# Kernel optimization log

Measured on AMD Instinct MI355X. Metric: run time of the kernel, lower is better.

## Reference

```python
import jax, jax.numpy as jnp
import numpy as np

NUM_HEAD = 16
DIM_MODEL = 1024
DIM_HEAD = DIM_MODEL // NUM_HEAD


def setup_inputs() -> dict:
    key = jax.random.key(0)
    ks = jax.random.split(key, 11)
    B, S, D = 2, 2048, DIM_MODEL
    w = lambda k: jax.random.normal(k, (D, D), dtype=jnp.float32) * 0.02
    b = lambda k: jax.random.normal(k, (D,), dtype=jnp.float32) * 0.02
    return {
        "Q": jax.random.normal(ks[0], (B, S, D), dtype=jnp.float32),
        "K": jax.random.normal(ks[1], (B, S, D), dtype=jnp.float32),
        "V": jax.random.normal(ks[2], (B, S, D), dtype=jnp.float32),
        "WQ": w(ks[3]), "bQ": b(ks[4]),
        "WK": w(ks[5]), "bK": b(ks[6]),
        "WV": w(ks[7]), "bV": b(ks[8]),
        "WO": w(ks[9]), "bO": b(ks[10]),
    }


def reference(Q, K, V, WQ, bQ, WK, bK, WV, bV, WO, bO):
    B, LQ, D = Q.shape
    LK, LV = K.shape[1], V.shape[1]
    H, dh = NUM_HEAD, DIM_HEAD
    # linear projections (torch Linear: x @ W.T + b)
    q = (Q @ WQ.T + bQ).reshape(B, H, LQ, dh)  # NOTE: raw reshape, no transpose (faithful to source)
    k = (K @ WK.T + bK).reshape(B, H, LK, dh)
    v = (V @ WV.T + bV).reshape(B, H, LV, dh)
    # scores: Q @ K^T, scaled by (dim_head ** 1) / 2 == dh/2 (faithful to source precedence)
    scores = jnp.einsum('bhqd,bhkd->bhqk', q, k) / (dh / 2)
    dist = jax.nn.softmax(scores, axis=-1)          # [B,H,LQ,LK]
    attn = jnp.einsum('bhqk,bhkd->bhqd', dist, v)   # [B,H,LQ,dh]
    attn = attn.reshape(B, LQ, H * dh)
    out = attn @ WO.T + bO
    return out, dist
```

## Files before the change

### kernel.cpp

```cpp
#include <hip/hip_runtime.h>
#include <stdint.h>

#define B_ 2
#define S_ 2048
#define D_ 1024
#define H_ 16
#define DH 64
#define BS_ (B_*S_)
#define QBLK 128
#define KBLK 128

typedef unsigned short u16;
typedef __attribute__((ext_vector_type(8))) __bf16 bf16x8;
typedef __attribute__((ext_vector_type(4))) float f32x4;

__device__ __forceinline__ u16 f2bf(float f){
  unsigned u = __float_as_uint(f);
  u += 0x7fffu + ((u >> 16) & 1u);
  return (u16)(u >> 16);
}
__device__ __forceinline__ float bf2f(u16 v){
  return __uint_as_float(((unsigned)v) << 16);
}

union pk8 { u16 a[8]; uint4 v; };

typedef __attribute__((address_space(1))) const unsigned gas_u32;
typedef __attribute__((address_space(3))) unsigned las_u32;
__device__ __forceinline__ void gload16(const void* g, void* l){
  __builtin_amdgcn_global_load_lds((gas_u32*)g, (las_u32*)l, 16, 0, 0);
}

__global__ __launch_bounds__(256) void cvt_kernel(
    const float* __restrict__ Q, const float* __restrict__ K, const float* __restrict__ V,
    const float* __restrict__ WQ, const float* __restrict__ WK,
    const float* __restrict__ WV, const float* __restrict__ WO,
    u16* Qc, u16* Kc, u16* Vc, u16* wq, u16* wk, u16* wv, u16* wo)
{
  const int b = blockIdx.x;
  const float* s; u16* d; size_t off;
  if (b < 6144){
    int t = b >> 11;
    s = t==0?Q:(t==1?K:V); d = t==0?Qc:(t==1?Kc:Vc);
    off = (size_t)(b & 2047)*2048;
  } else {
    int t = (b - 6144) >> 9;
    s = t==0?WQ:(t==1?WK:(t==2?WV:WO)); d = t==0?wq:(t==1?wk:(t==2?wv:wo));
    off = (size_t)((b - 6144) & 511)*2048;
  }
  const float* sp = s + off + (size_t)threadIdx.x*8;
  f32x4 v0 = __builtin_nontemporal_load((const f32x4*)sp);
  f32x4 v1 = __builtin_nontemporal_load((const f32x4*)(sp + 4));
  pk8 p;
  p.a[0]=f2bf(v0[0]); p.a[1]=f2bf(v0[1]); p.a[2]=f2bf(v0[2]); p.a[3]=f2bf(v0[3]);
  p.a[4]=f2bf(v1[0]); p.a[5]=f2bf(v1[1]); p.a[6]=f2bf(v1[2]); p.a[7]=f2bf(v1[3]);
  *(uint4*)(d + off + (size_t)threadIdx.x*8) = p.v;
}

template<int F32OUT>
__device__ __forceinline__ void gemm_body(
    const u16* __restrict__ A, const u16* __restrict__ Wt,
    const float* __restrict__ bias, void* __restrict__ Cout,
    int bm, int bn, int N, int K)
{
  const int tid = threadIdx.x, w = tid >> 6, lane = tid & 63;
  const int g = lane >> 4, c16 = lane & 15;
  const int wr = w >> 1, wc = w & 1;
  const int lr = lane >> 3, lg = lane & 7;
  const int gsrc = lg ^ (lr & 7);

  __shared__ alignas(16) u16 at[2][128*64];
  __shared__ alignas(16) u16 bt[2][128*64];

  f32x4 acc[4][4];
  #pragma unroll
  for (int mi = 0; mi < 4; ++mi)
    #pragma unroll
    for (int ni = 0; ni < 4; ++ni) acc[mi][ni] = (f32x4){0.f,0.f,0.f,0.f};

  auto stage = [&](int buf, int kt){
    #pragma unroll
    for (int i = 0; i < 4; ++i){
      const int r = w*32 + i*8 + lr;
      gload16(A + (size_t)(bm*128 + r)*K + kt + gsrc*8, at[buf] + (w*32 + i*8)*64);
    }
    #pragma unroll
    for (int i = 0; i < 4; ++i){
      const int r = w*32 + i*8 + lr;
      gload16(Wt + (size_t)(bn*128 + r)*K + kt + gsrc*8, bt[buf] + (w*32 + i*8)*64);
    }
  };

  stage(0, 0);
  __syncthreads();
  int cur = 0;
  for (int kt = 0; kt < K; kt += 64){
    if (kt + 64 < K) stage(cur ^ 1, kt + 64);
    #pragma unroll
    for (int ks = 0; ks < 2; ++ks){
      bf16x8 af[4], bfr[4];
      #pragma unroll
      for (int mi = 0; mi < 4; ++mi){
        const int row = wr*64 + mi*16 + c16;
        af[mi] = *(const bf16x8*)(at[cur] + row*64 + ((ks*4 + g) ^ (row & 7))*8);
      }
      #pragma unroll
      for (int ni = 0; ni < 4; ++ni){
        const int row = wc*64 + ni*16 + c16;
        bfr[ni] = *(const bf16x8*)(bt[cur] + row*64 + ((ks*4 + g) ^ (row & 7))*8);
      }
      #pragma unroll
      for (int mi = 0; mi < 4; ++mi)
        #pragma unroll
        for (int ni = 0; ni < 4; ++ni)
          acc[mi][ni] = __builtin_amdgcn_mfma_f32_16x16x32_bf16(
              af[mi], bfr[ni], acc[mi][ni], 0, 0, 0);
    }
    __syncthreads();
    cur ^= 1;
  }

  #pragma unroll
  for (int mi = 0; mi < 4; ++mi){
    const int row0 = bm*128 + wr*64 + mi*16 + g*4;
    #pragma unroll
    for (int ni = 0; ni < 4; ++ni){
      const int col = bn*128 + wc*64 + ni*16 + c16;
      const float bb = bias[col];
      #pragma unroll
      for (int r = 0; r < 4; ++r){
        float v = acc[mi][ni][r] + bb;
        if (F32OUT) __builtin_nontemporal_store(v, (float*)Cout + (size_t)(row0 + r)*N + col);
        else        ((u16*)Cout)[(size_t)(row0 + r)*N + col] = f2bf(v);
      }
    }
  }
}

__global__ __launch_bounds__(256) void qkv_gemm_kernel(
    const u16* __restrict__ A0, const u16* __restrict__ A1, const u16* __restrict__ A2,
    const u16* __restrict__ W0, const u16* __restrict__ W1, const u16* __restrict__ W2,
    const float* __restrict__ b0, const float* __restrict__ b1, const float* __restrict__ b2,
    u16* C0, u16* C1, u16* C2)
{
  const int t = blockIdx.z;
  const u16* A = t==0?A0:(t==1?A1:A2);
  const u16* W = t==0?W0:(t==1?W1:W2);
  const float* bb = t==0?b0:(t==1?b1:b2);
  u16* C = t==0?C0:(t==1?C1:C2);
  gemm_body<0>(A, W, bb, C, blockIdx.x, blockIdx.y, D_, D_);
}

__global__ __launch_bounds__(256) void out_gemm_kernel(
    const u16* __restrict__ A, const u16* __restrict__ W,
    const float* __restrict__ bias, float* __restrict__ C)
{
  gemm_body<1>(A, W, bias, C, blockIdx.x, blockIdx.y, D_, D_);
}

__global__ __launch_bounds__(256) void vtrans_kernel(
    const u16* __restrict__ vb, u16* __restrict__ vtb)
{
  const int kt = blockIdx.x, bh = blockIdx.y;
  __shared__ alignas(16) u16 t[64][80];
  const int tid = threadIdx.x;
  const u16* slab = vb + (size_t)bh*S_*DH + (size_t)kt*64*DH;
  #pragma unroll
  for (int j = 0; j < 2; ++j){
    const int r = j*32 + (tid >> 3), c = (tid & 7)*8;
    *(bf16x8*)(&t[r][c]) = *(const bf16x8*)(slab + (size_t)r*DH + c);
  }
  __syncthreads();
  u16* oslab = vtb + (size_t)bh*DH*S_ + (size_t)kt*64;
  #pragma unroll
  for (int j = 0; j < 2; ++j){
    const int dd = j*32 + (tid >> 3), k8 = (tid & 7)*8;
    pk8 u;
    #pragma unroll
    for (int e = 0; e < 8; ++e) u.a[e] = t[k8 + e][dd];
    *(uint4*)(oslab + (size_t)dd*S_ + k8) = u.v;
  }
}

__global__ __launch_bounds__(512, 4) void attn_kernel(
    const u16* __restrict__ qb, const u16* __restrict__ kb,
    const u16* __restrict__ vtb, float* __restrict__ dist,
    u16* __restrict__ attnb)
{
  const int vb_ = (blockIdx.x & 7)*64 + (blockIdx.x >> 3);
  const int qblk = vb_ & 15, bh = vb_ >> 4;

  const int tid = threadIdx.x, w = tid >> 6, lane = tid & 63;
  const int g = lane >> 4, c16 = lane & 15;
  const int lr = lane >> 3, lg = lane & 7;
  const int gsrc = lg ^ (lr & 7);
  const int lr4 = lane >> 4, lg4 = lane & 15;

  __shared__ alignas(16) u16 klds[128*64];
  __shared__ alignas(16) u16 vtlds[64*128];
  __shared__ alignas(16) u16 plds[8*16*128];

  const u16* qsl = qb  + (size_t)bh*S_*DH;
  const u16* ksl = kb  + (size_t)bh*S_*DH;
  const u16* vsl = vtb + (size_t)bh*DH*S_;

  const int q0 = qblk*QBLK + w*16;
  bf16x8 qf[2];
  #pragma unroll
  for (int ks = 0; ks < 2; ++ks)
    qf[ks] = *(const bf16x8*)(qsl + (size_t)(q0 + c16)*DH + ks*32 + g*8);

  const float cl = (1.0f/32.0f)*1.44269504f;
  float sum = 0.f;

  auto stageK = [&](int kt){
    #pragma unroll
    for (int i = 0; i < 2; ++i){
      const int r = w*16 + i*8 + lr;
      gload16(ksl + (size_t)(kt + r)*DH + gsrc*8, klds + (w*16 + i*8)*64);
    }
  };
  auto stageV = [&](int kt){
    #pragma unroll
    for (int i = 0; i < 2; ++i){
      const int d = w*8 + i*4 + lr4;
      const int gs = lg4 ^ (d & 15);
      gload16(vsl + (size_t)d*S_ + kt + gs*8, vtlds + (w*8 + i*4)*128);
    }
  };

  for (int kt = 0; kt < S_; kt += KBLK){
    stageK(kt);
    __syncthreads();
    #pragma unroll
    for (int ng = 0; ng < 2; ++ng){
      bf16x8 kf[4][2];
      f32x4 s[4];
      #pragma unroll
      for (int j = 0; j < 4; ++j){
        const int krow = (ng*4 + j)*16 + c16;
        kf[j][0] = *(const bf16x8*)(klds + krow*64 + ((0 + g) ^ (krow & 7))*8);
        kf[j][1] = *(const bf16x8*)(klds + krow*64 + ((4 + g) ^ (krow & 7))*8);
      }
      __builtin_amdgcn_s_setprio(1);
      #pragma unroll
      for (int j = 0; j < 4; ++j){
        s[j] = (f32x4){0.f,0.f,0.f,0.f};
        s[j] = __builtin_amdgcn_mfma_f32_16x16x32_bf16(kf[j][0], qf[0], s[j], 0, 0, 0);
      }
      #pragma unroll
      for (int j = 0; j < 4; ++j)
        s[j] = __builtin_amdgcn_mfma_f32_16x16x32_bf16(kf[j][1], qf[1], s[j], 0, 0, 0);
      __builtin_amdgcn_s_setprio(0);
      #pragma unroll
      for (int j = 0; j < 4; ++j)
        #pragma unroll
        for (int r = 0; r < 4; ++r) sum += exp2f(s[j][r]*cl);
    }
    __syncthreads();
  }
  sum += __shfl_xor(sum, 16, 64);
  sum += __shfl_xor(sum, 32, 64);
  const float inv = 1.0f/sum;

  f32x4 oacc[4];
  #pragma unroll
  for (int n2 = 0; n2 < 4; ++n2) oacc[n2] = (f32x4){0.f,0.f,0.f,0.f};

  float* drow0 = dist + ((size_t)bh*S_ + q0)*S_;
  const int rlane = lane >> 5;
  const int chunk = lane & 31;
  const int slotc = chunk >> 1, halfc = (chunk & 1)*4;

  for (int kt = 0; kt < S_; kt += KBLK){
    stageK(kt);
    stageV(kt);
    __syncthreads();
    #pragma unroll
    for (int ng = 0; ng < 2; ++ng){
      bf16x8 kf[4][2];
      f32x4 s[4];
      #pragma unroll
      for (int j = 0; j < 4; ++j){
        const int krow = (ng*4 + j)*16 + c16;
        kf[j][0] = *(const bf16x8*)(klds + krow*64 + ((0 + g) ^ (krow & 7))*8);
        kf[j][1] = *(const bf16x8*)(klds + krow*64 + ((4 + g) ^ (krow & 7))*8);
      }
      __builtin_amdgcn_s_setprio(1);
      #pragma unroll
      for (int j = 0; j < 4; ++j){
        s[j] = (f32x4){0.f,0.f,0.f,0.f};
        s[j] = __builtin_amdgcn_mfma_f32_16x16x32_bf16(kf[j][0], qf[0], s[j], 0, 0, 0);
      }
      #pragma unroll
      for (int j = 0; j < 4; ++j)
        s[j] = __builtin_amdgcn_mfma_f32_16x16x32_bf16(kf[j][1], qf[1], s[j], 0, 0, 0);
      __builtin_amdgcn_s_setprio(0);
      #pragma unroll
      for (int j = 0; j < 4; ++j){
        const int n = ng*4 + j;
        float p0 = exp2f(s[j][0]*cl)*inv, p1 = exp2f(s[j][1]*cl)*inv;
        float p2 = exp2f(s[j][2]*cl)*inv, p3 = exp2f(s[j][3]*cl)*inv;
        const int col = n*16 + g*4;
        const int slot = (col >> 3) ^ c16;
        unsigned lo = (unsigned)f2bf(p0) | ((unsigned)f2bf(p1) << 16);
        unsigned hi = (unsigned)f2bf(p2) | ((unsigned)f2bf(p3) << 16);
        uint2 pk2; pk2.x = lo; pk2.y = hi;
        *(uint2*)(plds + w*2048 + c16*128 + slot*8 + (g & 1)*4) = pk2;
      }
    }
    #pragma unroll
    for (int it = 0; it < 8; ++it){
      const int row = it*2 + rlane;
      const u16* src = plds + w*2048 + row*128 + (slotc ^ row)*8 + halfc;
      uint2 pv = *(const uint2*)src;
      f32x4 o;
      o[0] = bf2f((u16)(pv.x & 0xffffu));
      o[1] = bf2f((u16)(pv.x >> 16));
      o[2] = bf2f((u16)(pv.y & 0xffffu));
      o[3] = bf2f((u16)(pv.y >> 16));
      __builtin_nontemporal_store(o, (f32x4*)(drow0 + (size_t)row*S_ + kt + chunk*4));
    }
    #pragma unroll
    for (int kc = 0; kc < 4; ++kc){
      bf16x8 pf = *(const bf16x8*)(plds + w*2048 + c16*128 + ((kc*4 + g) ^ c16)*8);
      __builtin_amdgcn_s_setprio(1);
      #pragma unroll
      for (int n2 = 0; n2 < 4; ++n2){
        const int d = n2*16 + c16;
        bf16x8 vf = *(const bf16x8*)(vtlds + d*128 + ((kc*4 + g) ^ (d & 15))*8);
        oacc[n2] = __builtin_amdgcn_mfma_f32_16x16x32_bf16(pf, vf, oacc[n2], 0, 0, 0);
      }
      __builtin_amdgcn_s_setprio(0);
    }
    __syncthreads();
  }

  u16* asl = attnb + (size_t)bh*S_*DH;
  #pragma unroll
  for (int n2 = 0; n2 < 4; ++n2)
    #pragma unroll
    for (int r = 0; r < 4; ++r)
      __builtin_nontemporal_store(f2bf(oacc[n2][r]),
          asl + (size_t)(q0 + g*4 + r)*DH + n2*16 + c16);
}

extern "C" void kernel_launch(void* const* d_in, const int* in_sizes, int n_in,
                              void* d_out, int out_size, void* d_ws, size_t ws_size,
                              hipStream_t stream)
{
  const float* Q  = (const float*)d_in[0];
  const float* K  = (const float*)d_in[1];
  const float* V  = (const float*)d_in[2];
  const float* WQ = (const float*)d_in[3]; const float* bQ = (const float*)d_in[4];
  const float* WK = (const float*)d_in[5]; const float* bK = (const float*)d_in[6];
  const float* WV = (const float*)d_in[7]; const float* bV = (const float*)d_in[8];
  const float* WO = (const float*)d_in[9]; const float* bO = (const float*)d_in[10];

  float* out  = (float*)d_out;
  float* dist = out + (size_t)BS_*D_;

  char* ws = (char*)d_ws;
  u16* qb    = (u16*)(ws);
  u16* kb    = (u16*)(ws + (8u<<20));
  u16* vb    = (u16*)(ws + (16u<<20));
  u16* vtb   = (u16*)(ws + (24u<<20));
  u16* attnb = (u16*)(ws + (32u<<20));
  u16* Qc    = (u16*)(ws + (40u<<20));
  u16* Kc    = (u16*)(ws + (48u<<20));
  u16* Vc    = (u16*)(ws + (56u<<20));
  u16* wqb   = (u16*)(ws + (64u<<20));
  u16* wkb   = (u16*)(ws + (66u<<20));
  u16* wvb   = (u16*)(ws + (68u<<20));
  u16* wob   = (u16*)(ws + (70u<<20));

  cvt_kernel<<<8192, 256, 0, stream>>>(Q, K, V, WQ, WK, WV, WO,
                                       Qc, Kc, Vc, wqb, wkb, wvb, wob);

  qkv_gemm_kernel<<<dim3(BS_/128, D_/128, 3), 256, 0, stream>>>(
      Qc, Kc, Vc, wqb, wkb, wvb, bQ, bK, bV, qb, kb, vb);

  vtrans_kernel<<<dim3(S_/64, B_*H_), 256, 0, stream>>>(vb, vtb);

  attn_kernel<<<dim3((S_/QBLK)*(B_*H_)), 512, 0, stream>>>(qb, kb, vtb, dist, attnb);

  out_gemm_kernel<<<dim3(BS_/128, D_/128), 256, 0, stream>>>(attnb, wob, bO, out);
}
```

Before: 230.8 us.

## Fuse fp32-to-bf16 activation conversion into QKV GEMM A-tile loading

The separate conversion pass over Q, K and V is removed. The QKV GEMM now loads fp32 activation tiles into registers, converts them to bf16, and writes them swizzled into LDS, with the next tile's loads overlapping the current MFMA loop. This drops a full fp32 read and bf16 write/read round trip of the activations, at the cost of more registers and re-reading fp32 A once per N-block (8 times) instead of bf16.

```diff
diff --git a/kernel.cpp b/kernel.cpp
--- a/kernel.cpp
+++ b/kernel.cpp
@@ -32,22 +32,15 @@
 }
 
 __global__ __launch_bounds__(256) void cvt_kernel(
-    const float* __restrict__ Q, const float* __restrict__ K, const float* __restrict__ V,
     const float* __restrict__ WQ, const float* __restrict__ WK,
     const float* __restrict__ WV, const float* __restrict__ WO,
-    u16* Qc, u16* Kc, u16* Vc, u16* wq, u16* wk, u16* wv, u16* wo)
+    u16* wq, u16* wk, u16* wv, u16* wo)
 {
   const int b = blockIdx.x;
-  const float* s; u16* d; size_t off;
-  if (b < 6144){
-    int t = b >> 11;
-    s = t==0?Q:(t==1?K:V); d = t==0?Qc:(t==1?Kc:Vc);
-    off = (size_t)(b & 2047)*2048;
-  } else {
-    int t = (b - 6144) >> 9;
-    s = t==0?WQ:(t==1?WK:(t==2?WV:WO)); d = t==0?wq:(t==1?wk:(t==2?wv:wo));
-    off = (size_t)((b - 6144) & 511)*2048;
-  }
+  const int t = b >> 9;
+  const float* s = t==0?WQ:(t==1?WK:(t==2?WV:WO));
+  u16* d = t==0?wq:(t==1?wk:(t==2?wv:wo));
+  const size_t off = (size_t)(b & 511)*2048;
   const float* sp = s + off + (size_t)threadIdx.x*8;
   f32x4 v0 = __builtin_nontemporal_load((const f32x4*)sp);
   f32x4 v1 = __builtin_nontemporal_load((const f32x4*)(sp + 4));
@@ -57,9 +50,9 @@
   *(uint4*)(d + off + (size_t)threadIdx.x*8) = p.v;
 }
 
-template<int F32OUT>
+template<int F32OUT, int AF32>
 __device__ __forceinline__ void gemm_body(
-    const u16* __restrict__ A, const u16* __restrict__ Wt,
+    const void* __restrict__ Ap, const u16* __restrict__ Wt,
     const float* __restrict__ bias, void* __restrict__ Cout,
     int bm, int bn, int N, int K)
 {
@@ -78,12 +71,35 @@
     #pragma unroll
     for (int ni = 0; ni < 4; ++ni) acc[mi][ni] = (f32x4){0.f,0.f,0.f,0.f};
 
-  auto stage = [&](int buf, int kt){
+  f32x4 a0[4], a1[4];
+  auto loadA = [&](int kt){
+    #pragma unroll
+    for (int i = 0; i < 4; ++i){
+      const int id = tid + i*256, row = id >> 3, gi = id & 7;
+      const float* src = (const float*)Ap + (size_t)(bm*128 + row)*K + kt + gi*8;
+      a0[i] = __builtin_nontemporal_load((const f32x4*)src);
+      a1[i] = __builtin_nontemporal_load((const f32x4*)(src + 4));
+    }
+  };
+  auto writeA = [&](int buf){
+    #pragma unroll
+    for (int i = 0; i < 4; ++i){
+      const int id = tid + i*256, row = id >> 3, gi = id & 7;
+      pk8 p;
+      p.a[0]=f2bf(a0[i][0]); p.a[1]=f2bf(a0[i][1]); p.a[2]=f2bf(a0[i][2]); p.a[3]=f2bf(a0[i][3]);
+      p.a[4]=f2bf(a1[i][0]); p.a[5]=f2bf(a1[i][1]); p.a[6]=f2bf(a1[i][2]); p.a[7]=f2bf(a1[i][3]);
+      *(uint4*)(at[buf] + row*64 + ((gi ^ (row & 7)))*8) = p.v;
+    }
+  };
+  auto stageA = [&](int buf, int kt){
     #pragma unroll
     for (int i = 0; i < 4; ++i){
       const int r = w*32 + i*8 + lr;
-      gload16(A + (size_t)(bm*128 + r)*K + kt + gsrc*8, at[buf] + (w*32 + i*8)*64);
-    }
+      gload16((const u16*)Ap + (size_t)(bm*128 + r)*K + kt + gsrc*8,
+              at[buf] + (w*32 + i*8)*64);
+    }
+  };
+  auto stageB = [&](int buf, int kt){
     #pragma unroll
     for (int i = 0; i < 4; ++i){
       const int r = w*32 + i*8 + lr;
@@ -91,11 +107,16 @@
     }
   };
 
-  stage(0, 0);
+  if (AF32){ loadA(0); stageB(0, 0); writeA(0); }
+  else     { stageA(0, 0); stageB(0, 0); }
   __syncthreads();
   int cur = 0;
   for (int kt = 0; kt < K; kt += 64){
-    if (kt + 64 < K) stage(cur ^ 1, kt + 64);
+    const bool more = kt + 64 < K;
+    if (more){
+      if (AF32) loadA(kt + 64); else stageA(cur ^ 1, kt + 64);
+      stageB(cur ^ 1, kt + 64);
+    }
     #pragma unroll
     for (int ks = 0; ks < 2; ++ks){
       bf16x8 af[4], bfr[4];
@@ -116,6 +137,7 @@
           acc[mi][ni] = __builtin_amdgcn_mfma_f32_16x16x32_bf16(
               af[mi], bfr[ni], acc[mi][ni], 0, 0, 0);
     }
+    if (AF32 && more) writeA(cur ^ 1);
     __syncthreads();
     cur ^= 1;
   }
@@ -138,24 +160,24 @@
 }
 
 __global__ __launch_bounds__(256) void qkv_gemm_kernel(
-    const u16* __restrict__ A0, const u16* __restrict__ A1, const u16* __restrict__ A2,
+    const float* __restrict__ Q, const float* __restrict__ K, const float* __restrict__ V,
     const u16* __restrict__ W0, const u16* __restrict__ W1, const u16* __restrict__ W2,
     const float* __restrict__ b0, const float* __restrict__ b1, const float* __restrict__ b2,
     u16* C0, u16* C1, u16* C2)
 {
   const int t = blockIdx.z;
-  const u16* A = t==0?A0:(t==1?A1:A2);
+  const float* A = t==0?Q:(t==1?K:V);
   const u16* W = t==0?W0:(t==1?W1:W2);
   const float* bb = t==0?b0:(t==1?b1:b2);
   u16* C = t==0?C0:(t==1?C1:C2);
-  gemm_body<0>(A, W, bb, C, blockIdx.x, blockIdx.y, D_, D_);
+  gemm_body<0,1>(A, W, bb, C, blockIdx.x, blockIdx.y, D_, D_);
 }
 
 __global__ __launch_bounds__(256) void out_gemm_kernel(
     const u16* __restrict__ A, const u16* __restrict__ W,
     const float* __restrict__ bias, float* __restrict__ C)
 {
-  gemm_body<1>(A, W, bias, C, blockIdx.x, blockIdx.y, D_, D_);
+  gemm_body<1,0>(A, W, bias, C, blockIdx.x, blockIdx.y, D_, D_);
 }
 
 __global__ __launch_bounds__(256) void vtrans_kernel(
@@ -366,19 +388,15 @@
   u16* vb    = (u16*)(ws + (16u<<20));
   u16* vtb   = (u16*)(ws + (24u<<20));
   u16* attnb = (u16*)(ws + (32u<<20));
-  u16* Qc    = (u16*)(ws + (40u<<20));
-  u16* Kc    = (u16*)(ws + (48u<<20));
-  u16* Vc    = (u16*)(ws + (56u<<20));
-  u16* wqb   = (u16*)(ws + (64u<<20));
-  u16* wkb   = (u16*)(ws + (66u<<20));
-  u16* wvb   = (u16*)(ws + (68u<<20));
-  u16* wob   = (u16*)(ws + (70u<<20));
-
-  cvt_kernel<<<8192, 256, 0, stream>>>(Q, K, V, WQ, WK, WV, WO,
-                                       Qc, Kc, Vc, wqb, wkb, wvb, wob);
+  u16* wqb   = (u16*)(ws + (40u<<20));
+  u16* wkb   = (u16*)(ws + (42u<<20));
+  u16* wvb   = (u16*)(ws + (44u<<20));
+  u16* wob   = (u16*)(ws + (46u<<20));
+
+  cvt_kernel<<<2048, 256, 0, stream>>>(WQ, WK, WV, WO, wqb, wkb, wvb, wob);
 
   qkv_gemm_kernel<<<dim3(BS_/128, D_/128, 3), 256, 0, stream>>>(
-      Qc, Kc, Vc, wqb, wkb, wvb, bQ, bK, bV, qb, kb, vb);
+      Q, K, V, wqb, wkb, wvb, bQ, bK, bV, qb, kb, vb);
 
   vtrans_kernel<<<dim3(S_/64, B_*H_), 256, 0, stream>>>(vb, vtb);
 
```

New measurement: 262.1 us. +13.6%, slower.
